# Performance work log

Hardware: AMD Instinct MI355X
Metric: run time of the kernel (lower is better)

The kernel has to match this reference:

```python
import jax, jax.numpy as jnp
import numpy as np

N, T, D = 20000, 60, 20      # nodes, window length, input features
H = 128                      # lstm_hidden
G = 128                      # gnn_hidden
HEADS = 4
C = G // HEADS               # per-head channels (gnn_hidden // heads)
E = 320000                   # directed edges
OUT = 2
NEG_SLOPE = 0.2              # PyG GATConv leaky-relu slope


def setup_inputs() -> dict:
    key = jax.random.key(0)
    ks = jax.random.split(key, 16)
    s = lambda k, shape, sc=0.05: jax.random.normal(k, shape, jnp.float32) * sc
    return {
        "x_win": jax.random.normal(ks[0], (N, T, D), jnp.float32),
        "edge_index": jax.random.randint(ks[1], (2, E), 0, N),
        # LSTM (1 layer, PyTorch gate order i,f,g,o)
        "Wih": s(ks[2], (4 * H, D)),
        "Whh": s(ks[3], (4 * H, H)),
        "bih": s(ks[4], (4 * H,)),
        "bhh": s(ks[5], (4 * H,)),
        # GAT layer 1
        "W1": s(ks[6], (H, G)),
        "att_src1": s(ks[7], (HEADS, C)),
        "att_dst1": s(ks[8], (HEADS, C)),
        "b1": s(ks[9], (G,)),
        # GAT layer 2
        "W2": s(ks[10], (G, G)),
        "att_src2": s(ks[11], (HEADS, C)),
        "att_dst2": s(ks[12], (HEADS, C)),
        "b2": s(ks[13], (G,)),
        # linear head
        "Wh": s(ks[14], (G, OUT)),
        "bh": s(ks[15], (OUT,)),
    }


def _lstm_last(x, Wih, Whh, bih, bhh):
    """Single-layer LSTM over [N, T, D]; return last hidden state [N, H]."""
    n = x.shape[0]
    h0 = jnp.zeros((n, Whh.shape[1]), x.dtype)
    c0 = jnp.zeros_like(h0)
    b = bih + bhh

    def step(carry, xt):
        h, c = carry
        gates = xt @ Wih.T + h @ Whh.T + b
        i, f, g, o = jnp.split(gates, 4, axis=-1)
        c = jax.nn.sigmoid(f) * c + jax.nn.sigmoid(i) * jnp.tanh(g)
        h = jax.nn.sigmoid(o) * jnp.tanh(c)
        return (h, c), None

    (h, _), _ = jax.lax.scan(step, (h0, c0), jnp.swapaxes(x, 0, 1))
    return h


def _gat(x, src, dst, W, a_src, a_dst, bias):
    """PyG-style GATConv (self-loops already in src/dst), concat heads + bias."""
    n = x.shape[0]
    xh = (x @ W).reshape(n, HEADS, C)                 # [N, heads, C]
    asr = (xh * a_src[None]).sum(-1)                  # [N, heads]
    adt = (xh * a_dst[None]).sum(-1)                  # [N, heads]
    e = jax.nn.leaky_relu(asr[src] + adt[dst], NEG_SLOPE)   # [E+N, heads]
    # per-destination softmax (numerically stable segment softmax)
    emax = jax.ops.segment_max(e, dst, num_segments=n)
    ex = jnp.exp(e - emax[dst])
    denom = jax.ops.segment_sum(ex, dst, num_segments=n)
    alpha = ex / (denom[dst] + 1e-16)                 # [E+N, heads]
    out = jax.ops.segment_sum(alpha[:, :, None] * xh[src], dst, num_segments=n)
    return out.reshape(n, HEADS * C) + bias


def reference(x_win, edge_index, Wih, Whh, bih, bhh,
              W1, att_src1, att_dst1, b1,
              W2, att_src2, att_dst2, b2, Wh, bh):
    node = _lstm_last(x_win, Wih, Whh, bih, bhh)      # dropout = identity (eval)
    loops = jnp.arange(N, dtype=edge_index.dtype)
    src = jnp.concatenate([edge_index[0], loops])     # add self-loops (PyG default)
    dst = jnp.concatenate([edge_index[1], loops])
    h = jax.nn.elu(_gat(node, src, dst, W1, att_src1, att_dst1, b1))
    h = jax.nn.elu(_gat(h, src, dst, W2, att_src2, att_dst2, b2))
    return h @ Wh + bh                                # [N, 2]
```

## Files before the change

kernel.cpp:

```cpp
#include <hip/hip_runtime.h>
#include <hip/hip_bf16.h>

#define NN 20000
#define TT 60
#define DD 20
#define HH 128
#define KK 148
#define EE 320000
#define EA 340000
#define ZSTRIDE 168
#define MROWS 80

typedef unsigned short u16;
typedef unsigned int u32;
typedef __attribute__((ext_vector_type(8))) short bf16x8;
typedef __attribute__((ext_vector_type(4))) float f32x4;

#define LOG2E  1.44269504088896340f
#define LOG2E2 2.88539008177792681f

__device__ __forceinline__ float bf2f(u16 u){ return __uint_as_float(((u32)u)<<16); }
__device__ __forceinline__ u16 f2bf(float f){
  u32 x = __float_as_uint(f);
  return (u16)((x + 0x7FFFu + ((x >> 16) & 1u)) >> 16);
}
__device__ __forceinline__ u16 f2bf_cvt(float f){
  float r;
  asm("v_cvt_pk_bf16_f32 %0, %1, %2" : "=v"(r) : "v"(f), "v"(f));
  return (u16)__float_as_uint(r);
}

__global__ void prep_lstm_kernel(const float* __restrict__ Wih, const float* __restrict__ Whh,
                                 const float* __restrict__ bih, const float* __restrict__ bhh,
                                 u16* __restrict__ Wfrag){
  int idx = blockIdx.x*256 + threadIdx.x;
  if (idx >= 8*4*5*64*8) return;
  int j    = idx & 7;
  int lane = (idx >> 3) & 63;
  int rest = idx >> 9;
  int kt = rest % 5, q = (rest/5) & 3, wc = rest/20;
  int col = q*128 + wc*16 + (lane & 15);
  int k   = kt*32 + ((lane >> 4) & 3)*8 + j;
  float v = 0.f;
  if (k < DD)       v = Wih[(size_t)col*DD + k];
  else if (k < KK)  v = Whh[(size_t)col*HH + (k - DD)];
  else if (k == KK) v = bih[col] + bhh[col];
  v *= (q == 2) ? LOG2E2 : LOG2E;
  Wfrag[idx] = f2bf(v);
}

__global__ void prep_w_kernel(const float* __restrict__ W1, const float* __restrict__ W2,
                              u16* __restrict__ W1f, u16* __restrict__ W2f){
  int idx = blockIdx.x*256 + threadIdx.x;
  const float* W = W1; u16* Wf = W1f;
  if (idx >= 8*4*64*8){ idx -= 8*4*64*8; W = W2; Wf = W2f; }
  int j = idx & 7, lane = (idx>>3) & 63, kt = (idx>>9) & 3, ct = idx>>11;
  int col = ct*16 + (lane & 15);
  int k   = kt*32 + ((lane>>4) & 3)*8 + j;
  Wf[idx] = f2bf(W[(size_t)k*128 + col]);
}

__global__ __launch_bounds__(512, 2) void lstm_kernel(const float* __restrict__ xwin,
    const u16* __restrict__ Wfrag, u16* __restrict__ node_h){
  __shared__ u16 z[2][MROWS][ZSTRIDE];
  const int tid  = threadIdx.x;
  const int lane = tid & 63;
  const int wc   = tid >> 6;
  const int nb   = blockIdx.x * MROWS;
  const int l15  = lane & 15;
  const int quad = lane >> 4;

  bf16x8 B[4][5];
  {
    const bf16x8* bp = (const bf16x8*)Wfrag;
    #pragma unroll
    for (int q = 0; q < 4; q++)
      #pragma unroll
      for (int kt = 0; kt < 5; kt++)
        B[q][kt] = bp[(size_t)((wc*20 + q*5 + kt)*64 + lane)];
  }

  for (int i = tid; i < 2*MROWS*(ZSTRIDE/2); i += 512) ((u32*)(&z[0][0][0]))[i] = 0;

  const float* xp[4]; int nrow[4], ecol[4], vld[4];
  #pragma unroll
  for (int k2 = 0; k2 < 4; k2++){
    int s = tid + k2*512;
    vld[k2] = (s < MROWS*DD);
    int ss = vld[k2] ? s : 0;
    nrow[k2] = ss/DD; ecol[k2] = ss - nrow[k2]*DD;
    xp[k2] = xwin + (size_t)(nb + nrow[k2])*(TT*DD) + ecol[k2];
  }

  __syncthreads();
  #pragma unroll
  for (int k2 = 0; k2 < 4; k2++)
    if (vld[k2]) z[0][nrow[k2]][ecol[k2]] = f2bf_cvt(xp[k2][0]);
  if (tid < 2*MROWS){
    int b = tid >= MROWS, r = tid - b*MROWS;
    z[b][r][KK] = 0x3F80;
  }

  const f32x4 zf = {0.f, 0.f, 0.f, 0.f};
  f32x4 cst[5];
  #pragma unroll
  for (int mt = 0; mt < 5; mt++) cst[mt] = zf;
  __syncthreads();

  #pragma unroll 1
  for (int t = 0; t < TT; t++){
    const int cur = t & 1, nxt = cur ^ 1;
    const int pre = (t + 1 < TT);

    float xf[4];
    #pragma unroll
    for (int k2 = 0; k2 < 4; k2++)
      xf[k2] = (pre && vld[k2]) ? xp[k2][(t+1)*DD] : 0.f;

    auto load_A = [&](const int mt, bf16x8 A[5]){
      #pragma unroll
      for (int kt = 0; kt < 5; kt++)
        A[kt] = *(const bf16x8*)&z[cur][mt*16 + l15][kt*32 + quad*8];
    };
    auto chains = [&](const bf16x8 A[5], f32x4 acc[4]){
      __builtin_amdgcn_s_setprio(1);
      #pragma unroll
      for (int q = 0; q < 4; q++){
        f32x4 a = __builtin_amdgcn_mfma_f32_16x16x32_bf16(A[0], B[q][0], zf, 0,0,0);
        a = __builtin_amdgcn_mfma_f32_16x16x32_bf16(A[1], B[q][1], a, 0,0,0);
        a = __builtin_amdgcn_mfma_f32_16x16x32_bf16(A[2], B[q][2], a, 0,0,0);
        a = __builtin_amdgcn_mfma_f32_16x16x32_bf16(A[3], B[q][3], a, 0,0,0);
        a = __builtin_amdgcn_mfma_f32_16x16x32_bf16(A[4], B[q][4], a, 0,0,0);
        acc[q] = a;
      }
      __builtin_amdgcn_s_setprio(0);
    };
    auto act = [&](const f32x4 acc[4], const int mt){
      f32x4 cv = cst[mt];
      #pragma unroll
      for (int r = 0; r < 4; r++){
        float pi = __builtin_amdgcn_exp2f(-acc[0][r]);
        float pf = __builtin_amdgcn_exp2f(-acc[1][r]);
        float qg = __builtin_amdgcn_exp2f(-acc[2][r]);
        float po = __builtin_amdgcn_exp2f(-acc[3][r]);
        float part = (1.f - qg) * __builtin_amdgcn_rcpf((1.f + pi)*(1.f + qg));
        float sf   = __builtin_amdgcn_rcpf(1.f + pf);
        float cc   = fmaf(cv[r], sf, part);
        cv[r] = cc;
        float qc = __builtin_amdgcn_exp2f(-LOG2E2*cc);
        float h  = (1.f - qc) * __builtin_amdgcn_rcpf((1.f + po)*(1.f + qc));
        const int row = mt*16 + quad*4 + r;
        u16 hb = f2bf_cvt(h);
        z[nxt][row][DD + wc*16 + l15] = hb;
        if (t == TT-1)
          node_h[(size_t)(nb + row)*HH + wc*16 + l15] = hb;
      }
      cst[mt] = cv;
    };

    bf16x8 Aa[5], Ab[5];
    f32x4 acA[4], acB[4];
    load_A(0, Aa); chains(Aa, acA);
    load_A(1, Ab); chains(Ab, acB);  act(acA, 0);
    load_A(2, Aa); chains(Aa, acA);  act(acB, 1);
    load_A(3, Ab); chains(Ab, acB);  act(acA, 2);
    load_A(4, Aa); chains(Aa, acA);  act(acB, 3);
    act(acA, 4);

    if (pre){
      #pragma unroll
      for (int k2 = 0; k2 < 4; k2++)
        if (vld[k2]) z[nxt][nrow[k2]][ecol[k2]] = f2bf_cvt(xf[k2]);
    }
    __syncthreads();
  }
}

__global__ __launch_bounds__(256) void gemm_kernel(const u16* __restrict__ X,
    const u16* __restrict__ Wf, u16* __restrict__ Y){
  __shared__ u16 xs[32][136];
  const int tid = threadIdx.x, lane = tid & 63, w = tid >> 6;
  const int l15 = lane & 15, quad = lane >> 4;
  const int rb  = blockIdx.x*32;

  for (int c = tid; c < 512; c += 256){
    int row = c >> 4, cc = c & 15;
    *(bf16x8*)&xs[row][cc*8] = *(const bf16x8*)&X[(size_t)(rb+row)*128 + cc*8];
  }
  bf16x8 Bf[2][4];
  #pragma unroll
  for (int ct = 0; ct < 2; ct++)
    #pragma unroll
    for (int kt = 0; kt < 4; kt++)
      Bf[ct][kt] = *(const bf16x8*)&Wf[(size_t)((((2*w+ct)*4 + kt)*64 + lane))*8];
  __syncthreads();

  bf16x8 A[2][4];
  #pragma unroll
  for (int mt = 0; mt < 2; mt++)
    #pragma unroll
    for (int kt = 0; kt < 4; kt++)
      A[mt][kt] = *(const bf16x8*)&xs[mt*16 + l15][kt*32 + quad*8];

  const f32x4 zf = {0.f,0.f,0.f,0.f};
  #pragma unroll
  for (int mt = 0; mt < 2; mt++)
    #pragma unroll
    for (int ct = 0; ct < 2; ct++){
      f32x4 a = __builtin_amdgcn_mfma_f32_16x16x32_bf16(A[mt][0], Bf[ct][0], zf, 0,0,0);
      a = __builtin_amdgcn_mfma_f32_16x16x32_bf16(A[mt][1], Bf[ct][1], a, 0,0,0);
      a = __builtin_amdgcn_mfma_f32_16x16x32_bf16(A[mt][2], Bf[ct][2], a, 0,0,0);
      a = __builtin_amdgcn_mfma_f32_16x16x32_bf16(A[mt][3], Bf[ct][3], a, 0,0,0);
      #pragma unroll
      for (int r = 0; r < 4; r++)
        Y[(size_t)(rb + mt*16 + quad*4 + r)*128 + (2*w+ct)*16 + l15] = f2bf(a[r]);
    }
}

__global__ __launch_bounds__(256) void att_kernel(const u16* __restrict__ XH,
    const float* __restrict__ att_s, const float* __restrict__ att_d,
    float* __restrict__ asr, float* __restrict__ adt){
  __shared__ float as_[128], ad_[128];
  int tid = threadIdx.x;
  if (tid < 128){ as_[tid] = att_s[tid]; ad_[tid] = att_d[tid]; }
  __syncthreads();
  int n = blockIdx.x*64 + (tid>>2);
  int h = tid & 3;
  if (n >= NN) return;
  const u16* row = XH + (size_t)n*128 + h*32;
  float sv = 0.f, dv = 0.f;
  #pragma unroll
  for (int blk = 0; blk < 4; blk++){
    bf16x8 v = *(const bf16x8*)(row + blk*8);
    #pragma unroll
    for (int j = 0; j < 8; j++){
      float x = bf2f((u16)v[j]);
      sv = fmaf(x, as_[h*32 + blk*8 + j], sv);
      dv = fmaf(x, ad_[h*32 + blk*8 + j], dv);
    }
  }
  asr[n*4+h] = sv; adt[n*4+h] = dv;
}

__device__ __forceinline__ void edge_sd(int e, const int* src, const int* dst, int& s, int& d){
  if (e < EE){ s = src[e]; d = dst[e]; } else { s = e - EE; d = s; }
}

__global__ void deg_kernel(const int* __restrict__ src, const int* __restrict__ dst,
                           int* __restrict__ deg){
  int e = blockIdx.x*256 + threadIdx.x;
  if (e >= EA) return;
  int s, d; edge_sd(e, src, dst, s, d);
  atomicAdd(deg + d, 1);
}

#define SCB 80
__global__ __launch_bounds__(256) void psum_kernel(const int* __restrict__ deg,
                                                   int* __restrict__ psum){
  __shared__ int ws[4];
  int i = blockIdx.x*256 + threadIdx.x;
  int v = (i < NN) ? deg[i] : 0;
  #pragma unroll
  for (int off = 32; off > 0; off >>= 1) v += __shfl_down(v, off);
  if ((threadIdx.x & 63) == 0) ws[threadIdx.x >> 6] = v;
  __syncthreads();
  if (threadIdx.x == 0) psum[blockIdx.x] = ws[0]+ws[1]+ws[2]+ws[3];
}

__global__ void pscan_kernel(const int* __restrict__ psum, int* __restrict__ boff,
                             int* __restrict__ rowptr){
  if (threadIdx.x == 0){
    int acc = 0;
    for (int b = 0; b < SCB; b++){ boff[b] = acc; acc += psum[b]; }
    boff[SCB] = acc;
    rowptr[NN] = acc;
  }
}

__global__ __launch_bounds__(256) void rowptr_kernel(const int* __restrict__ deg,
    const int* __restrict__ boff, int* __restrict__ rowptr, int* __restrict__ cursor){
  __shared__ int buf[256];
  const int tid = threadIdx.x;
  int i = blockIdx.x*256 + tid;
  int v = (i < NN) ? deg[i] : 0;
  buf[tid] = v;
  __syncthreads();
  #pragma unroll
  for (int off = 1; off < 256; off <<= 1){
    int t = (tid >= off) ? buf[tid - off] : 0;
    __syncthreads();
    buf[tid] += t;
    __syncthreads();
  }
  if (i < NN){
    int excl = buf[tid] - v + boff[blockIdx.x];
    rowptr[i] = excl; cursor[i] = excl;
  }
}

__global__ void fill_kernel(const int* __restrict__ src, const int* __restrict__ dst,
                            int* __restrict__ cursor, int* __restrict__ elist){
  int e = blockIdx.x*256 + threadIdx.x;
  if (e >= EA) return;
  int s, d; edge_sd(e, src, dst, s, d);
  int pos = atomicAdd(cursor + d, 1);
  elist[pos] = s;
}

__global__ __launch_bounds__(512) void gat_kernel(const int* __restrict__ rowptr,
    const int* __restrict__ elist, const float* __restrict__ asr,
    const float* __restrict__ adt, const u16* __restrict__ XH,
    const float* __restrict__ bias, u16* __restrict__ out,
    const float* __restrict__ Wh, const float* __restrict__ bh,
    float* __restrict__ outf){
  const int tid = threadIdx.x, lane = tid & 63, w = tid >> 6;
  const int d = blockIdx.x*8 + w;
  const int r0 = rowptr[d], r1 = rowptr[d+1];
  const int h = lane >> 4;
  const int c = lane*2;
  float4 ad4 = *(const float4*)(adt + (size_t)d*4);
  const float adh = (h==0) ? ad4.x : (h==1) ? ad4.y : (h==2) ? ad4.z : ad4.w;

  float den = 0.f, accx = 0.f, accy = 0.f;
  int s_cur = elist[r0];
  float4 a_cur = *(const float4*)(asr + (size_t)s_cur*4);
  u32 pk_cur = ((const u32*)XH)[(size_t)s_cur*64 + lane];
  for (int idx = r0; idx < r1; idx++){
    int s_nxt = (idx+1 < r1) ? elist[idx+1] : s_cur;
    float4 a_nxt = *(const float4*)(asr + (size_t)s_nxt*4);
    u32 pk_nxt = ((const u32*)XH)[(size_t)s_nxt*64 + lane];
    float av = (h==0) ? a_cur.x : (h==1) ? a_cur.y : (h==2) ? a_cur.z : a_cur.w;
    float l = av + adh; l = l > 0.f ? l : 0.2f*l;
    float ex = __expf(l);
    den += ex;
    accx = fmaf(ex, bf2f((u16)pk_cur),       accx);
    accy = fmaf(ex, bf2f((u16)(pk_cur>>16)), accy);
    a_cur = a_nxt; pk_cur = pk_nxt; s_cur = s_nxt;
  }
  float rd = __builtin_amdgcn_rcpf(den);
  float vx = accx*rd + bias[c], vy = accy*rd + bias[c+1];
  vx = vx > 0.f ? vx : __expf(vx) - 1.f;
  vy = vy > 0.f ? vy : __expf(vy) - 1.f;

  if (Wh == nullptr){
    u32 pk = (u32)f2bf(vx) | ((u32)f2bf(vy) << 16);
    ((u32*)out)[(size_t)d*64 + lane] = pk;
  } else {
    float p0 = vx*Wh[c*2]   + vy*Wh[c*2+2];
    float p1 = vx*Wh[c*2+1] + vy*Wh[c*2+3];
    #pragma unroll
    for (int off = 32; off > 0; off >>= 1){
      p0 += __shfl_xor(p0, off);
      p1 += __shfl_xor(p1, off);
    }
    if (lane == 0){
      float2 o; o.x = p0 + bh[0]; o.y = p1 + bh[1];
      ((float2*)outf)[d] = o;
    }
  }
}

extern "C" void kernel_launch(void* const* d_in, const int* in_sizes, int n_in,
                              void* d_out, int out_size, void* d_ws, size_t ws_size,
                              hipStream_t stream){
  const float* xwin = (const float*)d_in[0];
  const int*   eidx = (const int*)d_in[1];
  const float* Wih  = (const float*)d_in[2];
  const float* Whh  = (const float*)d_in[3];
  const float* bih  = (const float*)d_in[4];
  const float* bhh  = (const float*)d_in[5];
  const float* W1   = (const float*)d_in[6];
  const float* as1  = (const float*)d_in[7];
  const float* ad1  = (const float*)d_in[8];
  const float* b1   = (const float*)d_in[9];
  const float* W2   = (const float*)d_in[10];
  const float* as2  = (const float*)d_in[11];
  const float* ad2  = (const float*)d_in[12];
  const float* b2   = (const float*)d_in[13];
  const float* Wh   = (const float*)d_in[14];
  const float* bh   = (const float*)d_in[15];
  const int* src = eidx;
  const int* dst = eidx + EE;

  char* ws = (char*)d_ws;
  size_t off = 0;
  auto alloc = [&](size_t bytes)->void*{
    void* p = ws + off; off += (bytes + 255) & ~(size_t)255; return p;
  };
  u16*   WfL   = (u16*)  alloc((size_t)8*4*5*64*8*sizeof(u16));
  u16*   W1f   = (u16*)  alloc((size_t)8*4*64*8*sizeof(u16));
  u16*   W2f   = (u16*)  alloc((size_t)8*4*64*8*sizeof(u16));
  u16*   nodeh = (u16*)  alloc((size_t)NN*128*sizeof(u16));
  u16*   xh    = (u16*)  alloc((size_t)NN*128*sizeof(u16));
  u16*   hbuf  = (u16*)  alloc((size_t)NN*128*sizeof(u16));
  float* asr   = (float*)alloc((size_t)NN*4*sizeof(float));
  float* adt   = (float*)alloc((size_t)NN*4*sizeof(float));
  int*   deg   = (int*)  alloc((size_t)NN*sizeof(int));
  int*   rowp  = (int*)  alloc((size_t)(NN+1)*sizeof(int));
  int*   curs  = (int*)  alloc((size_t)NN*sizeof(int));
  int*   psum  = (int*)  alloc((size_t)SCB*sizeof(int));
  int*   boff  = (int*)  alloc((size_t)(SCB+1)*sizeof(int));
  int*   elist = (int*)  alloc((size_t)EA*sizeof(int));
  (void)ws_size; (void)in_sizes; (void)n_in; (void)out_size;

  const int EGRID = (EA+255)/256;

  prep_lstm_kernel<<<(8*4*5*64*8+255)/256, 256, 0, stream>>>(Wih, Whh, bih, bhh, WfL);
  prep_w_kernel<<<(2*8*4*64*8+255)/256, 256, 0, stream>>>(W1, W2, W1f, W2f);
  hipMemsetAsync(deg, 0, (size_t)NN*sizeof(int), stream);
  deg_kernel<<<EGRID, 256, 0, stream>>>(src, dst, deg);
  psum_kernel<<<SCB, 256, 0, stream>>>(deg, psum);
  pscan_kernel<<<1, 64, 0, stream>>>(psum, boff, rowp);
  rowptr_kernel<<<SCB, 256, 0, stream>>>(deg, boff, rowp, curs);
  fill_kernel<<<EGRID, 256, 0, stream>>>(src, dst, curs, elist);

  lstm_kernel<<<NN/MROWS, 512, 0, stream>>>(xwin, WfL, nodeh);

  gemm_kernel<<<NN/32, 256, 0, stream>>>(nodeh, W1f, xh);
  att_kernel<<<(NN+63)/64, 256, 0, stream>>>(xh, as1, ad1, asr, adt);
  gat_kernel<<<NN/8, 512, 0, stream>>>(rowp, elist, asr, adt, xh, b1, hbuf,
                                       nullptr, nullptr, nullptr);
  gemm_kernel<<<NN/32, 256, 0, stream>>>(hbuf, W2f, xh);
  att_kernel<<<(NN+63)/64, 256, 0, stream>>>(xh, as2, ad2, asr, adt);
  gat_kernel<<<NN/8, 512, 0, stream>>>(rowp, elist, asr, adt, xh, b2, nullptr,
                                       Wh, bh, (float*)d_out);
}
```

Measured before the change: 516.5 us.

## Shrink LSTM blocks to 40 rows with 4 waves each owning two column tiles

Restructures the LSTM kernel to 256-thread blocks handling 40 nodes, padded to 48 rows in LDS. Each wave now holds B fragments for two 16-column tiles and walks three row tiles, instead of 8 waves each owning one column tile over 80 rows. The change doubles the block count (500 blocks), which spreads the sequential recurrence across more CUs. It also drops the manual double-buffered chain/activation interleave, and wastes MFMA work on 8 padding rows per block while raising register use per wave.

New measurement: 668.1 us. +29.3%, slower.

```diff
diff --git a/kernel.cpp b/kernel.cpp
--- a/kernel.cpp
+++ b/kernel.cpp
@@ -9,7 +9,8 @@
 #define EE 320000
 #define EA 340000
 #define ZSTRIDE 168
-#define MROWS 80
+#define MROWS 40
+#define ZROWS 48
 
 typedef unsigned short u16;
 typedef unsigned int u32;
@@ -38,8 +39,8 @@
   int j    = idx & 7;
   int lane = (idx >> 3) & 63;
   int rest = idx >> 9;
-  int kt = rest % 5, q = (rest/5) & 3, wc = rest/20;
-  int col = q*128 + wc*16 + (lane & 15);
+  int kt = rest % 5, q = (rest/5) & 3, g = rest/20;
+  int col = q*128 + g*16 + (lane & 15);
   int k   = kt*32 + ((lane >> 4) & 3)*8 + j;
   float v = 0.f;
   if (k < DD)       v = Wih[(size_t)col*DD + k];
@@ -60,9 +61,9 @@
   Wf[idx] = f2bf(W[(size_t)k*128 + col]);
 }
 
-__global__ __launch_bounds__(512, 2) void lstm_kernel(const float* __restrict__ xwin,
+__global__ __launch_bounds__(256, 2) void lstm_kernel(const float* __restrict__ xwin,
     const u16* __restrict__ Wfrag, u16* __restrict__ node_h){
-  __shared__ u16 z[2][MROWS][ZSTRIDE];
+  __shared__ u16 z[2][ZROWS][ZSTRIDE];
   const int tid  = threadIdx.x;
   const int lane = tid & 63;
   const int wc   = tid >> 6;
@@ -70,22 +71,24 @@
   const int l15  = lane & 15;
   const int quad = lane >> 4;
 
-  bf16x8 B[4][5];
+  bf16x8 B[2][4][5];
   {
     const bf16x8* bp = (const bf16x8*)Wfrag;
     #pragma unroll
-    for (int q = 0; q < 4; q++)
+    for (int ct = 0; ct < 2; ct++)
       #pragma unroll
-      for (int kt = 0; kt < 5; kt++)
-        B[q][kt] = bp[(size_t)((wc*20 + q*5 + kt)*64 + lane)];
-  }
-
-  for (int i = tid; i < 2*MROWS*(ZSTRIDE/2); i += 512) ((u32*)(&z[0][0][0]))[i] = 0;
+      for (int q = 0; q < 4; q++)
+        #pragma unroll
+        for (int kt = 0; kt < 5; kt++)
+          B[ct][q][kt] = bp[(size_t)(((wc*2+ct)*20 + q*5 + kt)*64 + lane)];
+  }
+
+  for (int i = tid; i < 2*ZROWS*(ZSTRIDE/2); i += 256) ((u32*)(&z[0][0][0]))[i] = 0;
 
   const float* xp[4]; int nrow[4], ecol[4], vld[4];
   #pragma unroll
   for (int k2 = 0; k2 < 4; k2++){
-    int s = tid + k2*512;
+    int s = tid + k2*256;
     vld[k2] = (s < MROWS*DD);
     int ss = vld[k2] ? s : 0;
     nrow[k2] = ss/DD; ecol[k2] = ss - nrow[k2]*DD;
@@ -96,15 +99,15 @@
   #pragma unroll
   for (int k2 = 0; k2 < 4; k2++)
     if (vld[k2]) z[0][nrow[k2]][ecol[k2]] = f2bf_cvt(xp[k2][0]);
-  if (tid < 2*MROWS){
-    int b = tid >= MROWS, r = tid - b*MROWS;
+  if (tid < 2*ZROWS){
+    int b = tid >= ZROWS, r = tid - b*ZROWS;
     z[b][r][KK] = 0x3F80;
   }
 
   const f32x4 zf = {0.f, 0.f, 0.f, 0.f};
-  f32x4 cst[5];
-  #pragma unroll
-  for (int mt = 0; mt < 5; mt++) cst[mt] = zf;
+  f32x4 cst[3][2];
+  #pragma unroll
+  for (int mt = 0; mt < 3; mt++){ cst[mt][0] = zf; cst[mt][1] = zf; }
   __syncthreads();
 
   #pragma unroll 1
@@ -117,55 +120,52 @@
     for (int k2 = 0; k2 < 4; k2++)
       xf[k2] = (pre && vld[k2]) ? xp[k2][(t+1)*DD] : 0.f;
 
-    auto load_A = [&](const int mt, bf16x8 A[5]){
+    #pragma unroll
+    for (int mt = 0; mt < 3; mt++){
+      bf16x8 A[5];
       #pragma unroll
       for (int kt = 0; kt < 5; kt++)
         A[kt] = *(const bf16x8*)&z[cur][mt*16 + l15][kt*32 + quad*8];
-    };
-    auto chains = [&](const bf16x8 A[5], f32x4 acc[4]){
-      __builtin_amdgcn_s_setprio(1);
+
       #pragma unroll
-      for (int q = 0; q < 4; q++){
-        f32x4 a = __builtin_amdgcn_mfma_f32_16x16x32_bf16(A[0], B[q][0], zf, 0,0,0);
-        a = __builtin_amdgcn_mfma_f32_16x16x32_bf16(A[1], B[q][1], a, 0,0,0);
-        a = __builtin_amdgcn_mfma_f32_16x16x32_bf16(A[2], B[q][2], a, 0,0,0);
-        a = __builtin_amdgcn_mfma_f32_16x16x32_bf16(A[3], B[q][3], a, 0,0,0);
-        a = __builtin_amdgcn_mfma_f32_16x16x32_bf16(A[4], B[q][4], a, 0,0,0);
-        acc[q] = a;
+      for (int ct = 0; ct < 2; ct++){
+        f32x4 acc[4];
+        __builtin_amdgcn_s_setprio(1);
+        #pragma unroll
+        for (int q = 0; q < 4; q++){
+          f32x4 a = __builtin_amdgcn_mfma_f32_16x16x32_bf16(A[0], B[ct][q][0], zf, 0,0,0);
+          a = __builtin_amdgcn_mfma_f32_16x16x32_bf16(A[1], B[ct][q][1], a, 0,0,0);
+          a = __builtin_amdgcn_mfma_f32_16x16x32_bf16(A[2], B[ct][q][2], a, 0,0,0);
+          a = __builtin_amdgcn_mfma_f32_16x16x32_bf16(A[3], B[ct][q][3], a, 0,0,0);
+          a = __builtin_amdgcn_mfma_f32_16x16x32_bf16(A[4], B[ct][q][4], a, 0,0,0);
+          acc[q] = a;
+        }
+        __builtin_amdgcn_s_setprio(0);
+
+        f32x4 cv = cst[mt][ct];
+        #pragma unroll
+        for (int r = 0; r < 4; r++){
+          float pi = __builtin_amdgcn_exp2f(-acc[0][r]);
+          float pf = __builtin_amdgcn_exp2f(-acc[1][r]);
+          float qg = __builtin_amdgcn_exp2f(-acc[2][r]);
+          float po = __builtin_amdgcn_exp2f(-acc[3][r]);
+          float part = (1.f - qg) * __builtin_amdgcn_rcpf((1.f + pi)*(1.f + qg));
+          float sf   = __builtin_amdgcn_rcpf(1.f + pf);
+          float cc   = fmaf(cv[r], sf, part);
+          cv[r] = cc;
+          float qc = __builtin_amdgcn_exp2f(-LOG2E2*cc);
+          float h  = (1.f - qc) * __builtin_amdgcn_rcpf((1.f + po)*(1.f + qc));
+          const int row = mt*16 + quad*4 + r;
+          if (row < MROWS){
+            u16 hb = f2bf_cvt(h);
+            z[nxt][row][DD + (wc*2+ct)*16 + l15] = hb;
+            if (t == TT-1)
+              node_h[(size_t)(nb + row)*HH + (wc*2+ct)*16 + l15] = hb;
+          }
+        }
+        cst[mt][ct] = cv;
       }
-      __builtin_amdgcn_s_setprio(0);
-    };
-    auto act = [&](const f32x4 acc[4], const int mt){
-      f32x4 cv = cst[mt];
-      #pragma unroll
-      for (int r = 0; r < 4; r++){
-        float pi = __builtin_amdgcn_exp2f(-acc[0][r]);
-        float pf = __builtin_amdgcn_exp2f(-acc[1][r]);
-        float qg = __builtin_amdgcn_exp2f(-acc[2][r]);
-        float po = __builtin_amdgcn_exp2f(-acc[3][r]);
-        float part = (1.f - qg) * __builtin_amdgcn_rcpf((1.f + pi)*(1.f + qg));
-        float sf   = __builtin_amdgcn_rcpf(1.f + pf);
-        float cc   = fmaf(cv[r], sf, part);
-        cv[r] = cc;
-        float qc = __builtin_amdgcn_exp2f(-LOG2E2*cc);
-        float h  = (1.f - qc) * __builtin_amdgcn_rcpf((1.f + po)*(1.f + qc));
-        const int row = mt*16 + quad*4 + r;
-        u16 hb = f2bf_cvt(h);
-        z[nxt][row][DD + wc*16 + l15] = hb;
-        if (t == TT-1)
-          node_h[(size_t)(nb + row)*HH + wc*16 + l15] = hb;
-      }
-      cst[mt] = cv;
-    };
-
-    bf16x8 Aa[5], Ab[5];
-    f32x4 acA[4], acB[4];
-    load_A(0, Aa); chains(Aa, acA);
-    load_A(1, Ab); chains(Ab, acB);  act(acA, 0);
-    load_A(2, Aa); chains(Aa, acA);  act(acB, 1);
-    load_A(3, Ab); chains(Ab, acB);  act(acA, 2);
-    load_A(4, Aa); chains(Aa, acA);  act(acB, 3);
-    act(acA, 4);
+    }
 
     if (pre){
       #pragma unroll
@@ -414,7 +414,7 @@
   rowptr_kernel<<<SCB, 256, 0, stream>>>(deg, boff, rowp, curs);
   fill_kernel<<<EGRID, 256, 0, stream>>>(src, dst, curs, elist);
 
-  lstm_kernel<<<NN/MROWS, 512, 0, stream>>>(xwin, WfL, nodeh);
+  lstm_kernel<<<NN/MROWS, 256, 0, stream>>>(xwin, WfL, nodeh);
 
   gemm_kernel<<<NN/32, 256, 0, stream>>>(nodeh, W1f, xh);
   att_kernel<<<(NN+63)/64, 256, 0, stream>>>(xh, as1, ad1, asr, adt);
```
